# Kernel tuning notes

Measured on AMD Instinct MI355X. Metric: run time of the kernel, lower is better.

The kernel has to match this reference:

```python
import jax, jax.numpy as jnp
import numpy as np
from jax import lax

FEAT = 16; STRIDE = 16; IMG = 256; K = 30; POOL = 7
NMS_TH = 0.85; TEMP = 0.07; B = 32; CLIP_DIM = 1024; PROJ = 256; NA = 9

def _anchors():
    scales = [8.0, 16.0, 32.0]; ratios = [0.5, 1.0, 2.0]
    A = []
    for i in range(FEAT):
        for j in range(FEAT):
            xc = (j + 0.5) * STRIDE; yc = (i + 0.5) * STRIDE
            for s in scales:
                for r in ratios:
                    w = s * r ** 0.5; h = s / r ** 0.5
                    A.append([xc - w / 2, yc - h / 2, xc + w / 2, yc + h / 2])
    return jnp.asarray(np.array(A, dtype=np.float32))  # [2304,4]

def _decode(reg, anchors):
    wh = anchors[:, 2:] - anchors[:, :2]; ctr = anchors[:, :2] + 0.5 * wh
    cx = reg[..., 0] * wh[:, 0] + ctr[:, 0]; cy = reg[..., 1] * wh[:, 1] + ctr[:, 1]
    pw = jnp.exp(reg[..., 2]) * wh[:, 0]; ph = jnp.exp(reg[..., 3]) * wh[:, 1]
    b = jnp.stack([cx - 0.5 * pw, cy - 0.5 * ph, cx + 0.5 * pw, cy + 0.5 * ph], -1)
    b = jnp.clip(b, 0.0, 256.0)
    x1, y1, x2, y2 = b[..., 0], b[..., 1], b[..., 2], b[..., 3]
    x2 = jnp.where(x2 - x1 < 1, x1 + 1, x2)
    y2 = jnp.where(y2 - y1 < 1, y1 + 1, y2)
    return jnp.stack([x1, y1, x2, y2], -1)

def _nms_keep(b):  # [K,4], already sorted by score desc
    x1, y1, x2, y2 = b[:, 0], b[:, 1], b[:, 2], b[:, 3]
    area = (x2 - x1) * (y2 - y1)
    iw = jnp.clip(jnp.minimum(x2[:, None], x2[None]) - jnp.maximum(x1[:, None], x1[None]), 0)
    ih = jnp.clip(jnp.minimum(y2[:, None], y2[None]) - jnp.maximum(y1[:, None], y1[None]), 0)
    inter = iw * ih
    iou = inter / (area[:, None] + area[None] - inter)
    idx = jnp.arange(K)
    def body(i, keep):
        supp = (idx > i) & (iou[i] > NMS_TH) & keep[i]
        return keep & ~supp
    return lax.fori_loop(0, K, body, jnp.ones(K, bool))

def _roi_align_mean(feats, bidx, rois):
    # roi_align(output 7x7, spatial_scale=1/16, sampling_ratio=1) then mean over bins
    N = rois.shape[0]; _, C, H, W = feats.shape
    sc = 1.0 / STRIDE
    x1, y1 = rois[:, 0] * sc, rois[:, 1] * sc
    rw = jnp.maximum(rois[:, 2] * sc - x1, 1.0); rh = jnp.maximum(rois[:, 3] * sc - y1, 1.0)
    g = jnp.arange(POOL, dtype=feats.dtype) + 0.5
    xs = x1[:, None] + g[None] * (rw / POOL)[:, None]  # [N,7]
    ys = y1[:, None] + g[None] * (rh / POOL)[:, None]
    X = jnp.broadcast_to(xs[:, None, :], (N, POOL, POOL))
    Y = jnp.broadcast_to(ys[:, :, None], (N, POOL, POOL))
    ok = (Y > -1) & (Y < H) & (X > -1) & (X < W)
    Xc = jnp.clip(X, 0, W - 1); Yc = jnp.clip(Y, 0, H - 1)
    x0 = jnp.floor(Xc).astype(jnp.int32); y0 = jnp.floor(Yc).astype(jnp.int32)
    x1i = jnp.minimum(x0 + 1, W - 1); y1i = jnp.minimum(y0 + 1, H - 1)
    lx = Xc - x0; ly = Yc - y0; hx = 1 - lx; hy = 1 - ly
    bN = bidx[:, None, None]
    f00 = feats[bN, :, y0, x0]; f01 = feats[bN, :, y0, x1i]  # [N,7,7,C]
    f10 = feats[bN, :, y1i, x0]; f11 = feats[bN, :, y1i, x1i]
    v = ((hy * hx)[..., None] * f00 + (hy * lx)[..., None] * f01
         + (ly * hx)[..., None] * f10 + (ly * lx)[..., None] * f11)
    v = v * ok[..., None]
    return v.mean(axis=(1, 2))  # [N,C]

def _roi_labels(gt_masks, bidx, rois):
    g = gt_masks[:, 0]  # [B,256,256]
    I = jnp.pad(jnp.cumsum(jnp.cumsum(g, 1), 2), ((0, 0), (1, 0), (1, 0)))  # integral image
    c = jnp.clip(rois.astype(jnp.int32), 0, IMG)
    x1, y1, x2, y2 = c[:, 0], c[:, 1], c[:, 2], c[:, 3]
    s = I[bidx, y2, x2] - I[bidx, y1, x2] - I[bidx, y2, x1] + I[bidx, y1, x1]
    cnt = (y2 - y1) * (x2 - x1)
    return jnp.where(cnt > 0, s / jnp.maximum(cnt, 1) > 0.5, False)

def _supcon(proj, labels, valid):
    nf = proj / jnp.clip(jnp.linalg.norm(proj, axis=1, keepdims=True), 1e-12)
    sim = (nf @ nf.T) / TEMP
    N = proj.shape[0]
    nd = ~jnp.eye(N, dtype=bool)
    vv = valid[:, None] & valid[None]
    pos = (labels[:, None] == labels[None]) & nd & vv
    vmask = nd & vv
    es = jnp.exp(sim)
    ratio = (es * pos).sum(1) / ((es * vmask).sum(1) + 1e-12)
    l = -jnp.log(ratio + 1e-12)
    active = valid & (pos.sum(1) > 0)
    cnt = active.sum()
    return jnp.where(cnt > 0, (l * active).sum() / jnp.maximum(cnt, 1), 0.0)

def _forward(clip_features, gt_masks, conv_w, conv_b, cls_w, cls_b, reg_w, reg_b,
             proj_w1, proj_b1, proj_w2, proj_b2):
    Bn = clip_features.shape[1]
    spatial = jnp.transpose(clip_features[1:], (1, 2, 0)).reshape(Bn, CLIP_DIM, FEAT, FEAT)
    x = jax.nn.relu(lax.conv_general_dilated(
        spatial, conv_w, (1, 1), 'SAME',
        dimension_numbers=('NCHW', 'OIHW', 'NCHW')) + conv_b[None, :, None, None])
    cls = jnp.einsum('bchw,ac->bahw', x, cls_w) + cls_b[None, :, None, None]
    reg = jnp.einsum('bchw,ac->bahw', x, reg_w) + reg_b[None, :, None, None]
    reg_p = reg.reshape(Bn, NA, 4, FEAT, FEAT).transpose(0, 3, 4, 1, 2).reshape(Bn, -1, 4)
    cls_p = cls.transpose(0, 2, 3, 1).reshape(Bn, -1)
    boxes = _decode(reg_p, _anchors())  # [B,2304,4]
    scores = jax.nn.sigmoid(cls_p)
    _, top_i = lax.top_k(scores, K)
    top_boxes = jnp.take_along_axis(boxes, top_i[..., None], axis=1)  # [B,K,4]
    keep = jax.vmap(_nms_keep)(top_boxes)  # [B,K]
    rois = lax.stop_gradient(top_boxes.reshape(-1, 4))  # torch roi_align/labels don't backprop thru roi coords
    valid = keep.reshape(-1)
    bidx = jnp.repeat(jnp.arange(Bn), K)
    pooled = _roi_align_mean(spatial, bidx, rois)  # [N,1024]
    h = jax.nn.relu(pooled @ proj_w1.T + proj_b1)
    proj = h @ proj_w2.T + proj_b2  # [N,256]
    labels = _roi_labels(gt_masks, bidx, rois)
    return _supcon(proj, labels, valid)

def setup_inputs() -> dict:
    key = jax.random.key(0)
    ks = jax.random.split(key, 8)
    s = 0.02
    return {
        'clip_features': jax.random.normal(ks[0], (257, B, CLIP_DIM), jnp.float32),
        'gt_masks': (jax.random.uniform(ks[1], (B, 1, IMG, IMG)) > 0.5).astype(jnp.float32),
        'conv_w': jax.random.normal(ks[2], (512, CLIP_DIM, 3, 3)) * s,
        'conv_b': jnp.zeros((512,)),
        'cls_w': jax.random.normal(ks[3], (NA, 512)) * s,
        'cls_b': jnp.zeros((NA,)),
        'reg_w': jax.random.normal(ks[4], (NA * 4, 512)) * s,
        'reg_b': jnp.zeros((NA * 4,)),
        'proj_w1': jax.random.normal(ks[5], (PROJ, CLIP_DIM)) * s,
        'proj_b1': jnp.zeros((PROJ,)),
        'proj_w2': jax.random.normal(ks[6], (PROJ, PROJ)) * s,
        'proj_b2': jnp.zeros((PROJ,)),
    }

def reference(clip_features, gt_masks, conv_w, conv_b, cls_w, cls_b, reg_w, reg_b,
              proj_w1, proj_b1, proj_w2, proj_b2):
    return _forward(clip_features, gt_masks, conv_w, conv_b, cls_w, cls_b, reg_w, reg_b,
                    proj_w1, proj_b1, proj_w2, proj_b2)
```

## Files before the change

kernel.cpp:

```cpp
#include <hip/hip_runtime.h>
#include <hip/hip_bf16.h>
#include <math.h>

typedef unsigned short u16;
typedef unsigned int u32;
typedef _Float16 f16;
typedef _Float16 f16x8 __attribute__((ext_vector_type(8)));
typedef float f32x4 __attribute__((ext_vector_type(4)));

#define BATCH 32
#define CIN   1024
#define COUT  512
#define NPOS  8192
#define K9    9216
#define KHALF 4608
#define TOPK  30
#define NROI  960
#define POOLN 7
#define IMG   256

#define O_XP0  0ull
#define O_XP1  4194304ull
#define O_CH   8388608ull
#define O_CL   12582912ull
#define O_WH   16777216ull
#define O_WL   19136512ull
#define O_Z    21495808ull
#define O_HW   21496064ull
#define O_SC   21519104ull
#define O_RG   21592832ull
#define O_ROI  21887744ull
#define O_VAL  21891584ull
#define O_LAB  21892544ull
#define O_W1T  21893504ull
#define O_W2T  22155648ull
#define WS_FLOATS 22221184ull
#define O_PO   0ull
#define O_NF   1474560ull
#define O_RL   1720320ull
#define O_RA   1721280ull

__device__ __forceinline__ void gl_lds16(const void* g, void* l) {
    __builtin_amdgcn_global_load_lds(
        (const __attribute__((address_space(1))) u32*)g,
        (__attribute__((address_space(3))) u32*)l,
        16, 0, 0);
}

__device__ inline void split16(float x, u16& h, u16& l) {
    f16 hv = (f16)x;
    f16 lv = (f16)(x - (float)hv);
    h = *(u16*)&hv;
    l = *(u16*)&lv;
}

#define NB_CLIP 8192
#define NB_W    2048
#define NB_Z    1
#define NB_HW   90
#define NB_W1T  1024
#define NB_W2T  256
__global__ __launch_bounds__(256)
void convert_all(const float* __restrict__ clip, const float* __restrict__ conv_w,
                 const float* __restrict__ cls_w, const float* __restrict__ reg_w,
                 const float* __restrict__ w1, const float* __restrict__ w2,
                 u16* __restrict__ CH, u16* __restrict__ CL,
                 u16* __restrict__ WH, u16* __restrict__ WL,
                 u16* __restrict__ Z, float* __restrict__ HW,
                 float* __restrict__ w1T, float* __restrict__ w2T) {
    __shared__ float wsh[2304];
    int bid = blockIdx.x, t = threadIdx.x;
    if (bid < NB_CLIP) {
        int tid = bid * 256 + t;
        int c4  = (tid & 255) * 4;
        int pos = (tid >> 8) & 255;
        int b   = tid >> 16;
        float4 v = *(const float4*)(clip + ((size_t)(1 + pos) * 32 + b) * 1024 + c4);
        float xs[4] = {v.x, v.y, v.z, v.w};
        ushort4 hh, ll;
        u16* hp = (u16*)&hh; u16* lp = (u16*)&ll;
#pragma unroll
        for (int q = 0; q < 4; ++q) split16(xs[q], hp[q], lp[q]);
        size_t o = ((size_t)(b * 256 + pos)) * 1024 + c4;
        *(ushort4*)(CH + o) = hh;
        *(ushort4*)(CL + o) = ll;
    } else if (bid < NB_CLIP + NB_W) {
        int bid2 = bid - NB_CLIP;
        int o = bid2 >> 2, cblk = bid2 & 3;
        const float* src = conv_w + (size_t)o * K9 + cblk * 2304;
        for (int i = t; i < 2304; i += 256) wsh[i] = src[i];
        __syncthreads();
#pragma unroll
        for (int p = 0; p < 9; ++p) {
            float x = wsh[t * 9 + p];
            u16 h, l;
            split16(x, h, l);
            size_t o2 = (size_t)o * K9 + p * 1024 + cblk * 256 + t;
            WH[o2] = h; WL[o2] = l;
        }
    } else if (bid < NB_CLIP + NB_W + NB_Z) {
        Z[t] = 0; Z[256 + t] = 0;
    } else if (bid < NB_CLIP + NB_W + NB_Z + NB_HW) {
        int tid2 = (bid - NB_CLIP - NB_W - NB_Z) * 256 + t;
        if (tid2 < 45 * 512) {
            int c = tid2 / 45, a = tid2 % 45;
            HW[tid2] = (a < 9) ? cls_w[a * 512 + c] : reg_w[(a - 9) * 512 + c];
        }
    } else if (bid < NB_CLIP + NB_W + NB_Z + NB_HW + NB_W1T) {
        int tid2 = (bid - NB_CLIP - NB_W - NB_Z - NB_HW) * 256 + t;
        int o = tid2 >> 10, c = tid2 & 1023;
        w1T[c * 256 + o] = w1[(size_t)o * 1024 + c];
    } else {
        int tid2 = (bid - NB_CLIP - NB_W - NB_Z - NB_HW - NB_W1T) * 256 + t;
        int o = tid2 >> 8, c = tid2 & 255;
        w2T[c * 256 + o] = w2[(size_t)o * 256 + c];
    }
}

__global__ __launch_bounds__(256, 2)
void conv_mfma(const u16* __restrict__ CH, const u16* __restrict__ CL,
               const u16* __restrict__ WH, const u16* __restrict__ WL,
               const u16* __restrict__ ZS,
               float* __restrict__ XP0, float* __restrict__ XP1) {
    __shared__ __align__(16) u16 Ah[8192];
    __shared__ __align__(16) u16 Al[8192];
    __shared__ __align__(16) u16 Bh[8192];
    __shared__ __align__(16) u16 Bl[8192];

    const int t = threadIdx.x;
    const int gid = blockIdx.x;
    const int nb = gid >> 7;
    const int g  = gid & 127;
    const int mb = g >> 1;
    const int ks = g & 1;
    const int ksOff = ks * KHALF;
    float* __restrict__ XP = ks ? XP1 : XP0;

    const int wave = t >> 6, lane = t & 63;

    int qA[2], siA[2], sjA[2], bA[2];
    const u16* srcBh[2];
    const u16* srcBl[2];
#pragma unroll
    for (int j = 0; j < 2; ++j) {
        int r = wave * 32 + j * 16 + (lane >> 2);
        int s = lane & 3;
        int q = s ^ ((r >> 1) & 3);
        qA[j] = q;
        int m = mb * 128 + r;
        bA[j] = m >> 8;
        int ij = m & 255;
        siA[j] = ij >> 4; sjA[j] = ij & 15;
        int o = nb * 128 + r;
        srcBh[j] = WH + (size_t)o * K9 + q * 8;
        srcBl[j] = WL + (size_t)o * K9 + q * 8;
    }

    const int wm = wave >> 1, wn = wave & 1;
    const int l16 = lane & 15, quad = lane >> 4;
    int offA[4], offB[4];
#pragma unroll
    for (int q = 0; q < 4; ++q) {
        int ar = wm * 64 + q * 16 + l16;
        offA[q] = ar * 32 + ((quad ^ ((ar >> 1) & 3)) << 3);
        int br = wn * 64 + q * 16 + l16;
        offB[q] = br * 32 + ((quad ^ ((br >> 1) & 3)) << 3);
    }

    f32x4 acc[4][4];
#pragma unroll
    for (int r = 0; r < 4; ++r)
#pragma unroll
        for (int c = 0; c < 4; ++c) acc[r][c] = (f32x4){0.f, 0.f, 0.f, 0.f};

    auto issue = [&](int it, int buf) {
        const int kg = ksOff + it * 32;
        const int p = kg >> 10;
        const int cb = kg & 1023;
        const int di = p / 3, dj = p - di * 3;
        const int base = buf << 12;
#pragma unroll
        for (int j = 0; j < 2; ++j) {
            int ii = siA[j] + di - 1, jj = sjA[j] + dj - 1;
            bool ok = ((unsigned)ii < 16u) && ((unsigned)jj < 16u);
            size_t aoff = ok ? ((((size_t)bA[j] << 8) + (size_t)(ii * 16 + jj)) << 10) + cb + qA[j] * 8
                             : 0;
            const u16* gah = ok ? CH + aoff : ZS;
            const u16* gal = ok ? CL + aoff : ZS;
            int lb = base + wave * 1024 + j * 512;
            gl_lds16(gah,           &Ah[lb]);
            gl_lds16(gal,           &Al[lb]);
            gl_lds16(srcBh[j] + kg, &Bh[lb]);
            gl_lds16(srcBl[j] + kg, &Bl[lb]);
        }
    };

    issue(0, 0);
    for (int it = 0; it < 144; ++it) {
        const int cur = it & 1;
        __syncthreads();
        if (it + 1 < 144) issue(it + 1, cur ^ 1);

        const int fb = cur << 12;
        f16x8 fah[4], fal[4], fbh[4], fbl[4];
#pragma unroll
        for (int x = 0; x < 4; ++x) {
            fah[x] = *(const f16x8*)&Ah[fb + offA[x]];
            fal[x] = *(const f16x8*)&Al[fb + offA[x]];
            fbh[x] = *(const f16x8*)&Bh[fb + offB[x]];
            fbl[x] = *(const f16x8*)&Bl[fb + offB[x]];
        }
#pragma unroll
        for (int tm = 0; tm < 4; ++tm)
#pragma unroll
            for (int tn = 0; tn < 4; ++tn) {
                acc[tm][tn] = __builtin_amdgcn_mfma_f32_16x16x32_f16(fal[tm], fbh[tn], acc[tm][tn], 0, 0, 0);
                acc[tm][tn] = __builtin_amdgcn_mfma_f32_16x16x32_f16(fah[tm], fbl[tn], acc[tm][tn], 0, 0, 0);
                acc[tm][tn] = __builtin_amdgcn_mfma_f32_16x16x32_f16(fah[tm], fbh[tn], acc[tm][tn], 0, 0, 0);
            }
    }

#pragma unroll
    for (int tm = 0; tm < 4; ++tm) {
        int mbase = mb * 128 + wm * 64 + tm * 16 + quad * 4;
#pragma unroll
        for (int tn = 0; tn < 4; ++tn) {
            int o = nb * 128 + wn * 64 + tn * 16 + l16;
#pragma unroll
            for (int r = 0; r < 4; ++r)
                XP[(size_t)(mbase + r) * COUT + o] = acc[tm][tn][r];
        }
    }
}

__global__ __launch_bounds__(64)
void heads_kernel(const float* __restrict__ XP0, const float* __restrict__ XP1,
                  const float* __restrict__ conv_b, const float* __restrict__ HW,
                  const float* __restrict__ cls_b, const float* __restrict__ reg_b,
                  float* __restrict__ scores, float* __restrict__ regs) {
    __shared__ float xs[512];
    int mm = blockIdx.x;
    int t = threadIdx.x;
#pragma unroll
    for (int q = 0; q < 8; ++q) {
        int c = t + 64 * q;
        xs[c] = fmaxf(XP0[(size_t)mm * COUT + c] + XP1[(size_t)mm * COUT + c] + conv_b[c], 0.f);
    }
    __syncthreads();
    if (t < 45) {
        float acc = (t < 9) ? cls_b[t] : reg_b[t - 9];
        for (int c = 0; c < 512; ++c) acc = fmaf(xs[c], HW[c * 45 + t], acc);
        int b = mm >> 8, cell = mm & 255;
        if (t < 9) {
            scores[(size_t)b * 2304 + cell * 9 + t] = 1.f / (1.f + expf(-acc));
        } else {
            int ch = t - 9;
            regs[((size_t)b * 2304 + cell * 9 + (ch >> 2)) * 4 + (ch & 3)] = acc;
        }
    }
}

__global__ __launch_bounds__(256)
void topk_nms(const float* __restrict__ scores, const float* __restrict__ regs,
              float* __restrict__ rois, float* __restrict__ valid) {
    __shared__ float sc[2304];
    __shared__ float wv[4];
    __shared__ int   wi[4];
    __shared__ int   sel[TOPK];
    __shared__ float bx[TOPK][4];
    __shared__ float iou[TOPK * TOPK];
    __shared__ float keepsh[TOPK];
    int b = blockIdx.x, t = threadIdx.x;
    for (int q = t; q < 2304; q += 256) sc[q] = scores[(size_t)b * 2304 + q];
    __syncthreads();

    for (int k = 0; k < TOPK; ++k) {
        float bv = -1e30f; int bi = 1 << 30;
#pragma unroll
        for (int q = 0; q < 9; ++q) {
            int idx = t * 9 + q;
            float v = sc[idx];
            if (v > bv || (v == bv && idx < bi)) { bv = v; bi = idx; }
        }
        for (int off = 32; off; off >>= 1) {
            float ov = __shfl_down(bv, off);
            int   oi = __shfl_down(bi, off);
            if (ov > bv || (ov == bv && oi < bi)) { bv = ov; bi = oi; }
        }
        int lane = t & 63, w = t >> 6;
        if (lane == 0) { wv[w] = bv; wi[w] = bi; }
        __syncthreads();
        if (t == 0) {
            float fv = wv[0]; int fi = wi[0];
            for (int q = 1; q < 4; ++q)
                if (wv[q] > fv || (wv[q] == fv && wi[q] < fi)) { fv = wv[q]; fi = wi[q]; }
            sel[k] = fi;
            sc[fi] = -1e38f;
        }
        __syncthreads();
    }

    if (t < TOPK) {
        int n = sel[t];
        int cell = n / 9, a = n % 9;
        int ci = cell >> 4, cj = cell & 15;
        int siid = a / 3, riid = a % 3;
        const double scl[3] = {8.0, 16.0, 32.0};
        const double rat[3] = {0.5, 1.0, 2.0};
        double s = scl[siid], r = rat[riid];
        double wD = s * sqrt(r), hD = s / sqrt(r);
        double xc = (cj + 0.5) * 16.0, yc = (ci + 0.5) * 16.0;
        float ax1 = (float)(xc - wD / 2), ay1 = (float)(yc - hD / 2);
        float ax2 = (float)(xc + wD / 2), ay2 = (float)(yc + hD / 2);
        float aw = ax2 - ax1, ah = ay2 - ay1;
        float ctrx = ax1 + 0.5f * aw, ctry = ay1 + 0.5f * ah;
        const float* rg = regs + ((size_t)b * 2304 + n) * 4;
        float cx = rg[0] * aw + ctrx;
        float cy = rg[1] * ah + ctry;
        float pw = expf(rg[2]) * aw;
        float ph = expf(rg[3]) * ah;
        float x1 = cx - 0.5f * pw, y1 = cy - 0.5f * ph;
        float x2 = cx + 0.5f * pw, y2 = cy + 0.5f * ph;
        x1 = fminf(fmaxf(x1, 0.f), 256.f);
        y1 = fminf(fmaxf(y1, 0.f), 256.f);
        x2 = fminf(fmaxf(x2, 0.f), 256.f);
        y2 = fminf(fmaxf(y2, 0.f), 256.f);
        if (x2 - x1 < 1.f) x2 = x1 + 1.f;
        if (y2 - y1 < 1.f) y2 = y1 + 1.f;
        bx[t][0] = x1; bx[t][1] = y1; bx[t][2] = x2; bx[t][3] = y2;
    }
    __syncthreads();
    if (t < TOPK * TOPK) {
        int ii = t / TOPK, jj = t % TOPK;
        float xi1 = bx[ii][0], yi1 = bx[ii][1], xi2 = bx[ii][2], yi2 = bx[ii][3];
        float xj1 = bx[jj][0], yj1 = bx[jj][1], xj2 = bx[jj][2], yj2 = bx[jj][3];
        float ai = (xi2 - xi1) * (yi2 - yi1), aj = (xj2 - xj1) * (yj2 - yj1);
        float iw = fmaxf(fminf(xi2, xj2) - fmaxf(xi1, xj1), 0.f);
        float ih = fmaxf(fminf(yi2, yj2) - fmaxf(yi1, yj1), 0.f);
        float inter = iw * ih;
        iou[t] = inter / (ai + aj - inter);
    }
    __syncthreads();
    if (t == 0) {
        bool keep[TOPK];
        for (int q = 0; q < TOPK; ++q) keep[q] = true;
        for (int iK = 0; iK < TOPK; ++iK) {
            if (!keep[iK]) continue;
            for (int jK = iK + 1; jK < TOPK; ++jK)
                if (keep[jK] && iou[iK * TOPK + jK] > 0.85f) keep[jK] = false;
        }
        for (int q = 0; q < TOPK; ++q) keepsh[q] = keep[q] ? 1.f : 0.f;
    }
    __syncthreads();
    if (t < TOPK) {
        int rr = b * TOPK + t;
        rois[rr * 4 + 0] = bx[t][0]; rois[rr * 4 + 1] = bx[t][1];
        rois[rr * 4 + 2] = bx[t][2]; rois[rr * 4 + 3] = bx[t][3];
        valid[rr] = keepsh[t];
    }
}

__global__ __launch_bounds__(256)
void align_labels(const float* __restrict__ clip, const float* __restrict__ gt,
                  const float* __restrict__ rois,
                  float* __restrict__ pooled, float* __restrict__ labels) {
    int bid = blockIdx.x, t = threadIdx.x;
    if (bid < NROI) {
        int r = bid;
        int b = r / TOPK;
        float rx1 = rois[r * 4 + 0] * 0.0625f, ry1 = rois[r * 4 + 1] * 0.0625f;
        float rw = fmaxf(rois[r * 4 + 2] * 0.0625f - rx1, 1.f);
        float rh = fmaxf(rois[r * 4 + 3] * 0.0625f - ry1, 1.f);
        float sx = rw / (float)POOLN, sy = rh / (float)POOLN;
        float acc[4] = {0.f, 0.f, 0.f, 0.f};
        for (int py = 0; py < POOLN; ++py) {
            float Y = ry1 + ((float)py + 0.5f) * sy;
            for (int px = 0; px < POOLN; ++px) {
                float Xx = rx1 + ((float)px + 0.5f) * sx;
                bool ok = (Y > -1.f) && (Y < 16.f) && (Xx > -1.f) && (Xx < 16.f);
                if (!ok) continue;
                float Xc = fminf(fmaxf(Xx, 0.f), 15.f);
                float Yc = fminf(fmaxf(Y, 0.f), 15.f);
                int x0 = (int)floorf(Xc), y0 = (int)floorf(Yc);
                int x1i = min(x0 + 1, 15), y1i = min(y0 + 1, 15);
                float lx = Xc - (float)x0, ly = Yc - (float)y0;
                float hx = 1.f - lx, hy = 1.f - ly;
                float w00 = hy * hx, w01 = hy * lx, w10 = ly * hx, w11 = ly * lx;
                const float* f00 = clip + (size_t)(1 + y0 * 16 + x0) * 32768 + (size_t)b * 1024;
                const float* f01 = clip + (size_t)(1 + y0 * 16 + x1i) * 32768 + (size_t)b * 1024;
                const float* f10 = clip + (size_t)(1 + y1i * 16 + x0) * 32768 + (size_t)b * 1024;
                const float* f11 = clip + (size_t)(1 + y1i * 16 + x1i) * 32768 + (size_t)b * 1024;
#pragma unroll
                for (int q = 0; q < 4; ++q) {
                    int c = t + 256 * q;
                    acc[q] += w00 * f00[c] + w01 * f01[c] + w10 * f10[c] + w11 * f11[c];
                }
            }
        }
#pragma unroll
        for (int q = 0; q < 4; ++q)
            pooled[(size_t)r * 1024 + t + 256 * q] = acc[q] / 49.f;
    } else {
        __shared__ float red[4];
        int r = bid - NROI;
        int b = r / TOPK;
        int x1 = min(max((int)rois[r * 4 + 0], 0), 256);
        int y1 = min(max((int)rois[r * 4 + 1], 0), 256);
        int x2 = min(max((int)rois[r * 4 + 2], 0), 256);
        int y2 = min(max((int)rois[r * 4 + 3], 0), 256);
        int cnt = (x2 - x1) * (y2 - y1);
        float s = 0.f;
        if (cnt > 0) {
            const float* g = gt + (size_t)b * (IMG * IMG);
            for (int yy = y1; yy < y2; ++yy) {
                const float* row = g + yy * IMG;
                for (int xx = x1 + t; xx < x2; xx += 256) s += row[xx];
            }
        }
        for (int off = 32; off; off >>= 1) s += __shfl_down(s, off);
        if ((t & 63) == 0) red[t >> 6] = s;
        __syncthreads();
        if (t == 0) {
            float tot = red[0] + red[1] + red[2] + red[3];
            labels[r] = (cnt > 0 && 2.f * tot > (float)cnt) ? 1.f : 0.f;
        }
    }
}

__global__ __launch_bounds__(256)
void fc_norm(const float* __restrict__ pooled, const float* __restrict__ w1T,
             const float* __restrict__ b1, const float* __restrict__ w2T,
             const float* __restrict__ b2, float* __restrict__ nf) {
    __shared__ float rows[4][1024];
    __shared__ float hsh[4][256];
    __shared__ float red[4];
    int r0 = blockIdx.x * 4, t = threadIdx.x;
    for (int q = 0; q < 4; ++q)
        for (int c = t; c < 1024; c += 256)
            rows[q][c] = pooled[(size_t)(r0 + q) * 1024 + c];
    __syncthreads();
    {
        float bv = b1[t];
        float acc[4] = {bv, bv, bv, bv};
        for (int c = 0; c < 1024; ++c) {
            float wv = w1T[c * 256 + t];
#pragma unroll
            for (int q = 0; q < 4; ++q) acc[q] = fmaf(rows[q][c], wv, acc[q]);
        }
#pragma unroll
        for (int q = 0; q < 4; ++q) hsh[q][t] = fmaxf(acc[q], 0.f);
    }
    __syncthreads();
    float pr[4];
    {
        float bv = b2[t];
        float acc[4] = {bv, bv, bv, bv};
        for (int c = 0; c < 256; ++c) {
            float wv = w2T[c * 256 + t];
#pragma unroll
            for (int q = 0; q < 4; ++q) acc[q] = fmaf(hsh[q][c], wv, acc[q]);
        }
#pragma unroll
        for (int q = 0; q < 4; ++q) pr[q] = acc[q];
    }
    for (int q = 0; q < 4; ++q) {
        float v = pr[q];
        float ss = v * v;
        for (int off = 32; off; off >>= 1) ss += __shfl_down(ss, off);
        if ((t & 63) == 0) red[t >> 6] = ss;
        __syncthreads();
        float tot = red[0] + red[1] + red[2] + red[3];
        float denom = fmaxf(sqrtf(tot), 1e-12f);
        nf[(size_t)(r0 + q) * 256 + t] = v / denom;
        __syncthreads();
    }
}

__global__ __launch_bounds__(256)
void supcon_rows(const float* __restrict__ nf, const float* __restrict__ labels,
                 const float* __restrict__ valid, float* __restrict__ rowl,
                 float* __restrict__ rowa) {
    __shared__ float my[256];
    __shared__ float labs[NROI], vals[NROI];
    __shared__ float wsa[4], wsp[4];
    __shared__ int wnp[4];
    int i = blockIdx.x, t = threadIdx.x;
    my[t] = nf[(size_t)i * 256 + t];
    for (int q = t; q < NROI; q += 256) { labs[q] = labels[q]; vals[q] = valid[q]; }
    __syncthreads();
    float vi = vals[i], li = labs[i];
    float sum_all = 0.f, sum_pos = 0.f;
    int np = 0;
    int w = t >> 6, lane = t & 63;
    float4 my4 = ((const float4*)my)[lane];
    if (vi > 0.5f) {
        for (int j = w; j < NROI; j += 4) {
            float4 v4 = ((const float4*)(nf + (size_t)j * 256))[lane];
            float p = my4.x * v4.x;
            p = fmaf(my4.y, v4.y, p);
            p = fmaf(my4.z, v4.z, p);
            p = fmaf(my4.w, v4.w, p);
#pragma unroll
            for (int off = 32; off; off >>= 1) p += __shfl_xor(p, off);
            if (j != i && vals[j] > 0.5f) {
                float e = expf(p / 0.07f);
                sum_all += e;
                if (labs[j] == li) { sum_pos += e; np++; }
            }
        }
    }
    if (lane == 0) { wsa[w] = sum_all; wsp[w] = sum_pos; wnp[w] = np; }
    __syncthreads();
    if (t == 0) {
        float sa = wsa[0] + wsa[1] + wsa[2] + wsa[3];
        float sp = wsp[0] + wsp[1] + wsp[2] + wsp[3];
        int tnp = wnp[0] + wnp[1] + wnp[2] + wnp[3];
        bool active = (vi > 0.5f) && (tnp > 0);
        float ratio = sp / (sa + 1e-12f);
        float l = -logf(ratio + 1e-12f);
        rowl[i] = active ? l : 0.f;
        rowa[i] = active ? 1.f : 0.f;
    }
}

__global__ __launch_bounds__(256)
void final_reduce(const float* __restrict__ rowl, const float* __restrict__ rowa,
                  float* __restrict__ out) {
    __shared__ float rl[4], ra[4];
    int t = threadIdx.x;
    float sl = 0.f, sa = 0.f;
    for (int q = t; q < NROI; q += 256) { sl += rowl[q]; sa += rowa[q]; }
    for (int off = 32; off; off >>= 1) { sl += __shfl_down(sl, off); sa += __shfl_down(sa, off); }
    if ((t & 63) == 0) { rl[t >> 6] = sl; ra[t >> 6] = sa; }
    __syncthreads();
    if (t == 0) {
        float L = rl[0] + rl[1] + rl[2] + rl[3];
        float A = ra[0] + ra[1] + ra[2] + ra[3];
        out[0] = (A > 0.f) ? (L / fmaxf(A, 1.f)) : 0.f;
    }
}

extern "C" void kernel_launch(void* const* d_in, const int* in_sizes, int n_in,
                              void* d_out, int out_size, void* d_ws, size_t ws_size,
                              hipStream_t stream) {
    const float* clip   = (const float*)d_in[0];
    const float* gt     = (const float*)d_in[1];
    const float* conv_w = (const float*)d_in[2];
    const float* conv_b = (const float*)d_in[3];
    const float* cls_w  = (const float*)d_in[4];
    const float* cls_b  = (const float*)d_in[5];
    const float* reg_w  = (const float*)d_in[6];
    const float* reg_b  = (const float*)d_in[7];
    const float* w1     = (const float*)d_in[8];
    const float* b1     = (const float*)d_in[9];
    const float* w2     = (const float*)d_in[10];
    const float* b2     = (const float*)d_in[11];

    if (ws_size < WS_FLOATS * sizeof(float)) return;

    float* ws  = (float*)d_ws;
    float* XP0 = ws + O_XP0;
    float* XP1 = ws + O_XP1;
    u16*   CH  = (u16*)(ws + O_CH);
    u16*   CL  = (u16*)(ws + O_CL);
    u16*   WHp = (u16*)(ws + O_WH);
    u16*   WLp = (u16*)(ws + O_WL);
    u16*   ZS  = (u16*)(ws + O_Z);
    float* HW  = ws + O_HW;
    float* SC  = ws + O_SC;
    float* RG  = ws + O_RG;
    float* ROI = ws + O_ROI;
    float* VAL = ws + O_VAL;
    float* LAB = ws + O_LAB;
    float* W1T = ws + O_W1T;
    float* W2T = ws + O_W2T;
    float* PO  = ws + O_PO;
    float* NF  = ws + O_NF;
    float* RL  = ws + O_RL;
    float* RA  = ws + O_RA;

    convert_all<<<NB_CLIP + NB_W + NB_Z + NB_HW + NB_W1T + NB_W2T, 256, 0, stream>>>(
        clip, conv_w, cls_w, reg_w, w1, w2, CH, CL, WHp, WLp, ZS, HW, W1T, W2T);
    conv_mfma<<<512, 256, 0, stream>>>(CH, CL, WHp, WLp, ZS, XP0, XP1);
    heads_kernel<<<NPOS, 64, 0, stream>>>(XP0, XP1, conv_b, HW, cls_b, reg_b, SC, RG);
    topk_nms<<<BATCH, 256, 0, stream>>>(SC, RG, ROI, VAL);
    align_labels<<<2 * NROI, 256, 0, stream>>>(clip, gt, ROI, PO, LAB);
    fc_norm<<<NROI / 4, 256, 0, stream>>>(PO, W1T, b1, W2T, b2, NF);
    supcon_rows<<<NROI, 256, 0, stream>>>(NF, LAB, VAL, RL, RA);
    final_reduce<<<1, 256, 0, stream>>>(RL, RA, (float*)d_out);
}
```

Measured before the change: 695.1 us.

## Stage per-image feature slices in LDS for RoI align; batch supcon rows

RoI align now runs one block per (image, 64-channel group). Each block loads the 16x16x64 feature slice into shared memory once and serves all 30 RoIs of that image from LDS, instead of gathering four global rows per bin for every RoI. Label computation moves into its own kernel. The supcon kernel now handles four anchor rows per block, so each neighbor row read from global memory is reused four times. The cost is 64KB of LDS per block, which lowers occupancy, plus one extra kernel launch.

```diff
diff --git a/kernel.cpp b/kernel.cpp
--- a/kernel.cpp
+++ b/kernel.cpp
@@ -361,18 +361,28 @@
 }
 
 __global__ __launch_bounds__(256)
-void align_labels(const float* __restrict__ clip, const float* __restrict__ gt,
-                  const float* __restrict__ rois,
-                  float* __restrict__ pooled, float* __restrict__ labels) {
-    int bid = blockIdx.x, t = threadIdx.x;
-    if (bid < NROI) {
-        int r = bid;
-        int b = r / TOPK;
+void align_img(const float* __restrict__ clip, const float* __restrict__ rois,
+               float* __restrict__ pooled) {
+    __shared__ float slice[16384];
+    int bid = blockIdx.x;
+    int b = bid >> 4, cg = bid & 15;
+    int t = threadIdx.x;
+    for (int idx = t; idx < 16384; idx += 256) {
+        int p = idx >> 6, c = idx & 63;
+        slice[idx] = clip[(size_t)(1 + p) * 32768 + (size_t)b * 1024 + cg * 64 + c];
+    }
+    __syncthreads();
+    int wv = t >> 6;
+    int ch = t & 63;
+    for (int rp = 0; rp < 8; ++rp) {
+        int rl = rp * 4 + wv;
+        if (rl >= TOPK) continue;
+        int r = b * TOPK + rl;
         float rx1 = rois[r * 4 + 0] * 0.0625f, ry1 = rois[r * 4 + 1] * 0.0625f;
         float rw = fmaxf(rois[r * 4 + 2] * 0.0625f - rx1, 1.f);
         float rh = fmaxf(rois[r * 4 + 3] * 0.0625f - ry1, 1.f);
         float sx = rw / (float)POOLN, sy = rh / (float)POOLN;
-        float acc[4] = {0.f, 0.f, 0.f, 0.f};
+        float acc = 0.f;
         for (int py = 0; py < POOLN; ++py) {
             float Y = ry1 + ((float)py + 0.5f) * sy;
             for (int px = 0; px < POOLN; ++px) {
@@ -386,44 +396,42 @@
                 float lx = Xc - (float)x0, ly = Yc - (float)y0;
                 float hx = 1.f - lx, hy = 1.f - ly;
                 float w00 = hy * hx, w01 = hy * lx, w10 = ly * hx, w11 = ly * lx;
-                const float* f00 = clip + (size_t)(1 + y0 * 16 + x0) * 32768 + (size_t)b * 1024;
-                const float* f01 = clip + (size_t)(1 + y0 * 16 + x1i) * 32768 + (size_t)b * 1024;
-                const float* f10 = clip + (size_t)(1 + y1i * 16 + x0) * 32768 + (size_t)b * 1024;
-                const float* f11 = clip + (size_t)(1 + y1i * 16 + x1i) * 32768 + (size_t)b * 1024;
-#pragma unroll
-                for (int q = 0; q < 4; ++q) {
-                    int c = t + 256 * q;
-                    acc[q] += w00 * f00[c] + w01 * f01[c] + w10 * f10[c] + w11 * f11[c];
-                }
+                float f00 = slice[(y0 * 16 + x0) * 64 + ch];
+                float f01 = slice[(y0 * 16 + x1i) * 64 + ch];
+                float f10 = slice[(y1i * 16 + x0) * 64 + ch];
+                float f11 = slice[(y1i * 16 + x1i) * 64 + ch];
+                acc += w00 * f00 + w01 * f01 + w10 * f10 + w11 * f11;
             }
         }
-#pragma unroll
-        for (int q = 0; q < 4; ++q)
-            pooled[(size_t)r * 1024 + t + 256 * q] = acc[q] / 49.f;
-    } else {
-        __shared__ float red[4];
-        int r = bid - NROI;
-        int b = r / TOPK;
-        int x1 = min(max((int)rois[r * 4 + 0], 0), 256);
-        int y1 = min(max((int)rois[r * 4 + 1], 0), 256);
-        int x2 = min(max((int)rois[r * 4 + 2], 0), 256);
-        int y2 = min(max((int)rois[r * 4 + 3], 0), 256);
-        int cnt = (x2 - x1) * (y2 - y1);
-        float s = 0.f;
-        if (cnt > 0) {
-            const float* g = gt + (size_t)b * (IMG * IMG);
-            for (int yy = y1; yy < y2; ++yy) {
-                const float* row = g + yy * IMG;
-                for (int xx = x1 + t; xx < x2; xx += 256) s += row[xx];
-            }
-        }
-        for (int off = 32; off; off >>= 1) s += __shfl_down(s, off);
-        if ((t & 63) == 0) red[t >> 6] = s;
-        __syncthreads();
-        if (t == 0) {
-            float tot = red[0] + red[1] + red[2] + red[3];
-            labels[r] = (cnt > 0 && 2.f * tot > (float)cnt) ? 1.f : 0.f;
-        }
+        pooled[(size_t)r * 1024 + cg * 64 + ch] = acc / 49.f;
+    }
+}
+
+__global__ __launch_bounds__(256)
+void labels_k(const float* __restrict__ gt, const float* __restrict__ rois,
+              float* __restrict__ labels) {
+    __shared__ float red[4];
+    int r = blockIdx.x, t = threadIdx.x;
+    int b = r / TOPK;
+    int x1 = min(max((int)rois[r * 4 + 0], 0), 256);
+    int y1 = min(max((int)rois[r * 4 + 1], 0), 256);
+    int x2 = min(max((int)rois[r * 4 + 2], 0), 256);
+    int y2 = min(max((int)rois[r * 4 + 3], 0), 256);
+    int cnt = (x2 - x1) * (y2 - y1);
+    float s = 0.f;
+    if (cnt > 0) {
+        const float* g = gt + (size_t)b * (IMG * IMG);
+        for (int yy = y1; yy < y2; ++yy) {
+            const float* row = g + yy * IMG;
+            for (int xx = x1 + t; xx < x2; xx += 256) s += row[xx];
+        }
+    }
+    for (int off = 32; off; off >>= 1) s += __shfl_down(s, off);
+    if ((t & 63) == 0) red[t >> 6] = s;
+    __syncthreads();
+    if (t == 0) {
+        float tot = red[0] + red[1] + red[2] + red[3];
+        labels[r] = (cnt > 0 && 2.f * tot > (float)cnt) ? 1.f : 0.f;
     }
 }
 
@@ -477,49 +485,64 @@
 }
 
 __global__ __launch_bounds__(256)
-void supcon_rows(const float* __restrict__ nf, const float* __restrict__ labels,
-                 const float* __restrict__ valid, float* __restrict__ rowl,
-                 float* __restrict__ rowa) {
-    __shared__ float my[256];
+void supcon_rows4(const float* __restrict__ nf, const float* __restrict__ labels,
+                  const float* __restrict__ valid, float* __restrict__ rowl,
+                  float* __restrict__ rowa) {
+    __shared__ float my[4][256];
     __shared__ float labs[NROI], vals[NROI];
-    __shared__ float wsa[4], wsp[4];
-    __shared__ int wnp[4];
-    int i = blockIdx.x, t = threadIdx.x;
-    my[t] = nf[(size_t)i * 256 + t];
+    __shared__ float wsa[4][4], wsp[4][4];
+    __shared__ int wnp[4][4];
+    int i0 = blockIdx.x * 4, t = threadIdx.x;
+#pragma unroll
+    for (int iq = 0; iq < 4; ++iq) my[iq][t] = nf[(size_t)(i0 + iq) * 256 + t];
     for (int q = t; q < NROI; q += 256) { labs[q] = labels[q]; vals[q] = valid[q]; }
     __syncthreads();
-    float vi = vals[i], li = labs[i];
-    float sum_all = 0.f, sum_pos = 0.f;
-    int np = 0;
     int w = t >> 6, lane = t & 63;
-    float4 my4 = ((const float4*)my)[lane];
-    if (vi > 0.5f) {
-        for (int j = w; j < NROI; j += 4) {
-            float4 v4 = ((const float4*)(nf + (size_t)j * 256))[lane];
-            float p = my4.x * v4.x;
-            p = fmaf(my4.y, v4.y, p);
-            p = fmaf(my4.z, v4.z, p);
-            p = fmaf(my4.w, v4.w, p);
+    float4 my4[4];
+    float vi[4], li[4];
+#pragma unroll
+    for (int iq = 0; iq < 4; ++iq) {
+        my4[iq] = ((const float4*)my[iq])[lane];
+        vi[iq] = vals[i0 + iq];
+        li[iq] = labs[i0 + iq];
+    }
+    float sa[4] = {0.f, 0.f, 0.f, 0.f}, sp[4] = {0.f, 0.f, 0.f, 0.f};
+    int np[4] = {0, 0, 0, 0};
+    for (int j = w; j < NROI; j += 4) {
+        float4 v4 = ((const float4*)(nf + (size_t)j * 256))[lane];
+        float vj = vals[j], lj = labs[j];
+#pragma unroll
+        for (int iq = 0; iq < 4; ++iq) {
+            float p = my4[iq].x * v4.x;
+            p = fmaf(my4[iq].y, v4.y, p);
+            p = fmaf(my4[iq].z, v4.z, p);
+            p = fmaf(my4[iq].w, v4.w, p);
 #pragma unroll
             for (int off = 32; off; off >>= 1) p += __shfl_xor(p, off);
-            if (j != i && vals[j] > 0.5f) {
+            if (vi[iq] > 0.5f && j != i0 + iq && vj > 0.5f) {
                 float e = expf(p / 0.07f);
-                sum_all += e;
-                if (labs[j] == li) { sum_pos += e; np++; }
+                sa[iq] += e;
+                if (lj == li[iq]) { sp[iq] += e; np[iq]++; }
             }
         }
     }
-    if (lane == 0) { wsa[w] = sum_all; wsp[w] = sum_pos; wnp[w] = np; }
+    if (lane == 0) {
+#pragma unroll
+        for (int iq = 0; iq < 4; ++iq) { wsa[iq][w] = sa[iq]; wsp[iq][w] = sp[iq]; wnp[iq][w] = np[iq]; }
+    }
     __syncthreads();
     if (t == 0) {
-        float sa = wsa[0] + wsa[1] + wsa[2] + wsa[3];
-        float sp = wsp[0] + wsp[1] + wsp[2] + wsp[3];
-        int tnp = wnp[0] + wnp[1] + wnp[2] + wnp[3];
-        bool active = (vi > 0.5f) && (tnp > 0);
-        float ratio = sp / (sa + 1e-12f);
-        float l = -logf(ratio + 1e-12f);
-        rowl[i] = active ? l : 0.f;
-        rowa[i] = active ? 1.f : 0.f;
+#pragma unroll
+        for (int iq = 0; iq < 4; ++iq) {
+            float s_a = wsa[iq][0] + wsa[iq][1] + wsa[iq][2] + wsa[iq][3];
+            float s_p = wsp[iq][0] + wsp[iq][1] + wsp[iq][2] + wsp[iq][3];
+            int tnp = wnp[iq][0] + wnp[iq][1] + wnp[iq][2] + wnp[iq][3];
+            bool active = (vi[iq] > 0.5f) && (tnp > 0);
+            float ratio = s_p / (s_a + 1e-12f);
+            float l = -logf(ratio + 1e-12f);
+            rowl[i0 + iq] = active ? l : 0.f;
+            rowa[i0 + iq] = active ? 1.f : 0.f;
+        }
     }
 }
 
@@ -584,8 +607,9 @@
     conv_mfma<<<512, 256, 0, stream>>>(CH, CL, WHp, WLp, ZS, XP0, XP1);
     heads_kernel<<<NPOS, 64, 0, stream>>>(XP0, XP1, conv_b, HW, cls_b, reg_b, SC, RG);
     topk_nms<<<BATCH, 256, 0, stream>>>(SC, RG, ROI, VAL);
-    align_labels<<<2 * NROI, 256, 0, stream>>>(clip, gt, ROI, PO, LAB);
+    align_img<<<512, 256, 0, stream>>>(clip, ROI, PO);
+    labels_k<<<NROI, 256, 0, stream>>>(gt, ROI, LAB);
     fc_norm<<<NROI / 4, 256, 0, stream>>>(PO, W1T, b1, W2T, b2, NF);
-    supcon_rows<<<NROI, 256, 0, stream>>>(NF, LAB, VAL, RL, RA);
+    supcon_rows4<<<NROI / 4, 256, 0, stream>>>(NF, LAB, VAL, RL, RA);
     final_reduce<<<1, 256, 0, stream>>>(RL, RA, (float*)d_out);
 }
```

New measurement: 869.1 us. 25.0% more time.

## Stage per-image feature slices in LDS for ROI align and split supcon rows

Applied to the files above, without the earlier changes.

ROI align now launches one block per (image, 64-channel group). Each block loads the 16x16x64 feature slice into shared memory once and computes all 30 ROIs of that image from LDS, instead of each ROI block gathering bilinear taps from global memory. The labels computation moves to its own kernel. The supcon row kernel is split into two halves per row, with the loss finalisation moved into the final reduce, to double parallelism. The LDS slice is 64KB per block, which limits occupancy, and adds one more kernel launch.

```diff
diff --git a/kernel.cpp b/kernel.cpp
--- a/kernel.cpp
+++ b/kernel.cpp
@@ -37,8 +37,7 @@
 #define WS_FLOATS 22221184ull
 #define O_PO   0ull
 #define O_NF   1474560ull
-#define O_RL   1720320ull
-#define O_RA   1721280ull
+#define O_PS   1720320ull
 
 __device__ __forceinline__ void gl_lds16(const void* g, void* l) {
     __builtin_amdgcn_global_load_lds(
@@ -361,18 +360,28 @@
 }
 
 __global__ __launch_bounds__(256)
-void align_labels(const float* __restrict__ clip, const float* __restrict__ gt,
-                  const float* __restrict__ rois,
-                  float* __restrict__ pooled, float* __restrict__ labels) {
-    int bid = blockIdx.x, t = threadIdx.x;
-    if (bid < NROI) {
-        int r = bid;
-        int b = r / TOPK;
+void align_img(const float* __restrict__ clip, const float* __restrict__ rois,
+               float* __restrict__ pooled) {
+    __shared__ float slice[16384];
+    int bid = blockIdx.x;
+    int b = bid >> 4, cg = bid & 15;
+    int t = threadIdx.x;
+    for (int idx = t; idx < 16384; idx += 256) {
+        int p = idx >> 6, c = idx & 63;
+        slice[idx] = clip[(size_t)(1 + p) * 32768 + (size_t)b * 1024 + cg * 64 + c];
+    }
+    __syncthreads();
+    int wv = t >> 6;
+    int ch = t & 63;
+    for (int rp = 0; rp < 8; ++rp) {
+        int rl = rp * 4 + wv;
+        if (rl >= TOPK) continue;
+        int r = b * TOPK + rl;
         float rx1 = rois[r * 4 + 0] * 0.0625f, ry1 = rois[r * 4 + 1] * 0.0625f;
         float rw = fmaxf(rois[r * 4 + 2] * 0.0625f - rx1, 1.f);
         float rh = fmaxf(rois[r * 4 + 3] * 0.0625f - ry1, 1.f);
         float sx = rw / (float)POOLN, sy = rh / (float)POOLN;
-        float acc[4] = {0.f, 0.f, 0.f, 0.f};
+        float acc = 0.f;
         for (int py = 0; py < POOLN; ++py) {
             float Y = ry1 + ((float)py + 0.5f) * sy;
             for (int px = 0; px < POOLN; ++px) {
@@ -386,44 +395,42 @@
                 float lx = Xc - (float)x0, ly = Yc - (float)y0;
                 float hx = 1.f - lx, hy = 1.f - ly;
                 float w00 = hy * hx, w01 = hy * lx, w10 = ly * hx, w11 = ly * lx;
-                const float* f00 = clip + (size_t)(1 + y0 * 16 + x0) * 32768 + (size_t)b * 1024;
-                const float* f01 = clip + (size_t)(1 + y0 * 16 + x1i) * 32768 + (size_t)b * 1024;
-                const float* f10 = clip + (size_t)(1 + y1i * 16 + x0) * 32768 + (size_t)b * 1024;
-                const float* f11 = clip + (size_t)(1 + y1i * 16 + x1i) * 32768 + (size_t)b * 1024;
-#pragma unroll
-                for (int q = 0; q < 4; ++q) {
-                    int c = t + 256 * q;
-                    acc[q] += w00 * f00[c] + w01 * f01[c] + w10 * f10[c] + w11 * f11[c];
-                }
+                float f00 = slice[(y0 * 16 + x0) * 64 + ch];
+                float f01 = slice[(y0 * 16 + x1i) * 64 + ch];
+                float f10 = slice[(y1i * 16 + x0) * 64 + ch];
+                float f11 = slice[(y1i * 16 + x1i) * 64 + ch];
+                acc += w00 * f00 + w01 * f01 + w10 * f10 + w11 * f11;
             }
         }
-#pragma unroll
-        for (int q = 0; q < 4; ++q)
-            pooled[(size_t)r * 1024 + t + 256 * q] = acc[q] / 49.f;
-    } else {
-        __shared__ float red[4];
-        int r = bid - NROI;
-        int b = r / TOPK;
-        int x1 = min(max((int)rois[r * 4 + 0], 0), 256);
-        int y1 = min(max((int)rois[r * 4 + 1], 0), 256);
-        int x2 = min(max((int)rois[r * 4 + 2], 0), 256);
-        int y2 = min(max((int)rois[r * 4 + 3], 0), 256);
-        int cnt = (x2 - x1) * (y2 - y1);
-        float s = 0.f;
-        if (cnt > 0) {
-            const float* g = gt + (size_t)b * (IMG * IMG);
-            for (int yy = y1; yy < y2; ++yy) {
-                const float* row = g + yy * IMG;
-                for (int xx = x1 + t; xx < x2; xx += 256) s += row[xx];
-            }
-        }
-        for (int off = 32; off; off >>= 1) s += __shfl_down(s, off);
-        if ((t & 63) == 0) red[t >> 6] = s;
-        __syncthreads();
-        if (t == 0) {
-            float tot = red[0] + red[1] + red[2] + red[3];
-            labels[r] = (cnt > 0 && 2.f * tot > (float)cnt) ? 1.f : 0.f;
-        }
+        pooled[(size_t)r * 1024 + cg * 64 + ch] = acc / 49.f;
+    }
+}
+
+__global__ __launch_bounds__(256)
+void labels_k(const float* __restrict__ gt, const float* __restrict__ rois,
+              float* __restrict__ labels) {
+    __shared__ float red[4];
+    int r = blockIdx.x, t = threadIdx.x;
+    int b = r / TOPK;
+    int x1 = min(max((int)rois[r * 4 + 0], 0), 256);
+    int y1 = min(max((int)rois[r * 4 + 1], 0), 256);
+    int x2 = min(max((int)rois[r * 4 + 2], 0), 256);
+    int y2 = min(max((int)rois[r * 4 + 3], 0), 256);
+    int cnt = (x2 - x1) * (y2 - y1);
+    float s = 0.f;
+    if (cnt > 0) {
+        const float* g = gt + (size_t)b * (IMG * IMG);
+        for (int yy = y1; yy < y2; ++yy) {
+            const float* row = g + yy * IMG;
+            for (int xx = x1 + t; xx < x2; xx += 256) s += row[xx];
+        }
+    }
+    for (int off = 32; off; off >>= 1) s += __shfl_down(s, off);
+    if ((t & 63) == 0) red[t >> 6] = s;
+    __syncthreads();
+    if (t == 0) {
+        float tot = red[0] + red[1] + red[2] + red[3];
+        labels[r] = (cnt > 0 && 2.f * tot > (float)cnt) ? 1.f : 0.f;
     }
 }
 
@@ -477,14 +484,14 @@
 }
 
 __global__ __launch_bounds__(256)
-void supcon_rows(const float* __restrict__ nf, const float* __restrict__ labels,
-                 const float* __restrict__ valid, float* __restrict__ rowl,
-                 float* __restrict__ rowa) {
+void supcon_half(const float* __restrict__ nf, const float* __restrict__ labels,
+                 const float* __restrict__ valid, float* __restrict__ PS) {
     __shared__ float my[256];
     __shared__ float labs[NROI], vals[NROI];
     __shared__ float wsa[4], wsp[4];
     __shared__ int wnp[4];
-    int i = blockIdx.x, t = threadIdx.x;
+    int bid = blockIdx.x, t = threadIdx.x;
+    int i = bid >> 1, half = bid & 1;
     my[t] = nf[(size_t)i * 256 + t];
     for (int q = t; q < NROI; q += 256) { labs[q] = labels[q]; vals[q] = valid[q]; }
     __syncthreads();
@@ -493,8 +500,9 @@
     int np = 0;
     int w = t >> 6, lane = t & 63;
     float4 my4 = ((const float4*)my)[lane];
+    int j0 = half * 480, j1 = j0 + 480;
     if (vi > 0.5f) {
-        for (int j = w; j < NROI; j += 4) {
+        for (int j = j0 + w; j < j1; j += 4) {
             float4 v4 = ((const float4*)(nf + (size_t)j * 256))[lane];
             float p = my4.x * v4.x;
             p = fmaf(my4.y, v4.y, p);
@@ -515,23 +523,30 @@
         float sa = wsa[0] + wsa[1] + wsa[2] + wsa[3];
         float sp = wsp[0] + wsp[1] + wsp[2] + wsp[3];
         int tnp = wnp[0] + wnp[1] + wnp[2] + wnp[3];
-        bool active = (vi > 0.5f) && (tnp > 0);
+        PS[(size_t)i * 6 + half * 3 + 0] = sa;
+        PS[(size_t)i * 6 + half * 3 + 1] = sp;
+        PS[(size_t)i * 6 + half * 3 + 2] = (float)tnp;
+    }
+}
+
+__global__ __launch_bounds__(256)
+void final_reduce2(const float* __restrict__ PS, const float* __restrict__ valid,
+                   float* __restrict__ out) {
+    __shared__ float rl[4], ra[4];
+    int t = threadIdx.x;
+    float sl = 0.f, sc = 0.f;
+    for (int i = t; i < NROI; i += 256) {
+        float sa = PS[(size_t)i * 6 + 0] + PS[(size_t)i * 6 + 3];
+        float sp = PS[(size_t)i * 6 + 1] + PS[(size_t)i * 6 + 4];
+        float np = PS[(size_t)i * 6 + 2] + PS[(size_t)i * 6 + 5];
+        bool active = (valid[i] > 0.5f) && (np > 0.5f);
         float ratio = sp / (sa + 1e-12f);
         float l = -logf(ratio + 1e-12f);
-        rowl[i] = active ? l : 0.f;
-        rowa[i] = active ? 1.f : 0.f;
-    }
-}
-
-__global__ __launch_bounds__(256)
-void final_reduce(const float* __restrict__ rowl, const float* __restrict__ rowa,
-                  float* __restrict__ out) {
-    __shared__ float rl[4], ra[4];
-    int t = threadIdx.x;
-    float sl = 0.f, sa = 0.f;
-    for (int q = t; q < NROI; q += 256) { sl += rowl[q]; sa += rowa[q]; }
-    for (int off = 32; off; off >>= 1) { sl += __shfl_down(sl, off); sa += __shfl_down(sa, off); }
-    if ((t & 63) == 0) { rl[t >> 6] = sl; ra[t >> 6] = sa; }
+        sl += active ? l : 0.f;
+        sc += active ? 1.f : 0.f;
+    }
+    for (int off = 32; off; off >>= 1) { sl += __shfl_down(sl, off); sc += __shfl_down(sc, off); }
+    if ((t & 63) == 0) { rl[t >> 6] = sl; ra[t >> 6] = sc; }
     __syncthreads();
     if (t == 0) {
         float L = rl[0] + rl[1] + rl[2] + rl[3];
@@ -576,16 +591,16 @@
     float* W2T = ws + O_W2T;
     float* PO  = ws + O_PO;
     float* NF  = ws + O_NF;
-    float* RL  = ws + O_RL;
-    float* RA  = ws + O_RA;
+    float* PS  = ws + O_PS;
 
     convert_all<<<NB_CLIP + NB_W + NB_Z + NB_HW + NB_W1T + NB_W2T, 256, 0, stream>>>(
         clip, conv_w, cls_w, reg_w, w1, w2, CH, CL, WHp, WLp, ZS, HW, W1T, W2T);
     conv_mfma<<<512, 256, 0, stream>>>(CH, CL, WHp, WLp, ZS, XP0, XP1);
     heads_kernel<<<NPOS, 64, 0, stream>>>(XP0, XP1, conv_b, HW, cls_b, reg_b, SC, RG);
     topk_nms<<<BATCH, 256, 0, stream>>>(SC, RG, ROI, VAL);
-    align_labels<<<2 * NROI, 256, 0, stream>>>(clip, gt, ROI, PO, LAB);
+    align_img<<<512, 256, 0, stream>>>(clip, ROI, PO);
+    labels_k<<<NROI, 256, 0, stream>>>(gt, ROI, LAB);
     fc_norm<<<NROI / 4, 256, 0, stream>>>(PO, W1T, b1, W2T, b2, NF);
-    supcon_rows<<<NROI, 256, 0, stream>>>(NF, LAB, VAL, RL, RA);
-    final_reduce<<<1, 256, 0, stream>>>(RL, RA, (float*)d_out);
-}
+    supcon_half<<<2 * NROI, 256, 0, stream>>>(NF, LAB, VAL, PS);
+    final_reduce2<<<1, 256, 0, stream>>>(PS, VAL, (float*)d_out);
+}
```

Result: no change. 681.9 us (-1.9%).
